# Kernel tuning notes

Measured on AMD Instinct MI355X. Metric: run time of the kernel, lower is better.

The kernel has to match this reference:

```python
import jax, jax.numpy as jnp
import numpy as np

N = 20000      # num nodes
E = 320000     # num edges (avg degree 16)
R = 8          # num relations
D = 256        # input_dim / hidden dim
L = 6          # num_layers
EE = 32        # edge_embed_dim
B = 64         # batch size
K = 32         # num_negative + 1


def _layer_norm(x, g, b, eps=1e-5):
    mu = jnp.mean(x, axis=-1, keepdims=True)
    var = jnp.var(x, axis=-1, keepdims=True)
    return (x - mu) * jax.lax.rsqrt(var + eps) * g + b


def setup_inputs() -> dict:
    key = jax.random.key(0)
    ks = jax.random.split(key, 10)
    edge_index = jax.random.randint(ks[0], (2, E), 0, N)
    edge_type = jax.random.randint(ks[1], (E,), 0, R)
    edge_embed = jax.random.normal(ks[2], (E, EE), dtype=jnp.float32)
    src = jax.random.randint(ks[3], (B, K), 0, N)
    tgt = jax.random.randint(ks[4], (B, K), 0, N)
    rel = jax.random.randint(ks[5], (B, K), 0, R)
    batch = jnp.stack([src, tgt, rel], axis=-1)  # [B, K, 3]
    s = 1.0 / np.sqrt(D)
    W = jax.random.normal(ks[6], (L, R, D, D), dtype=jnp.float32) * s      # per-relation weights
    Wself = jax.random.normal(ks[7], (L, D, D), dtype=jnp.float32) * s     # self-loop weights
    We = jax.random.normal(ks[8], (L, EE, D), dtype=jnp.float32) * (1.0 / np.sqrt(EE))  # edge-embed proj (stage add)
    gamma = jnp.ones((L, D), dtype=jnp.float32)
    beta = jnp.zeros((L, D), dtype=jnp.float32)
    rel_emb = jax.random.normal(ks[9], (R, D), dtype=jnp.float32) * s      # DistMult relation embedding
    return dict(edge_index=edge_index, edge_type=edge_type, edge_embed=edge_embed,
                batch=batch, W=W, Wself=Wself, We=We, gamma=gamma, beta=beta,
                rel_emb=rel_emb)


def reference(edge_index, edge_type, edge_embed, batch, W, Wself, We, gamma, beta, rel_emb):
    src, dst = edge_index[0], edge_index[1]
    # mean aggregation denominator: in-degree per node (over all relations)
    deg = jnp.clip(jax.ops.segment_sum(jnp.ones((E,), jnp.float32), dst, num_segments=N), 1.0)
    # segment id combining relation and destination node -> aggregate-then-transform trick
    seg = edge_type * N + dst
    x = jnp.ones((N, D), dtype=jnp.float32)
    for l in range(L):
        # stage 'add': message = x[src] + proj(edge_embed)
        msg = x[src] + edge_embed @ We[l]                                  # [E, D]
        agg = jax.ops.segment_sum(msg, seg, num_segments=R * N).reshape(R, N, D)
        h = jnp.einsum('rnd,rdf->nf', agg, W[l]) / deg[:, None] + x @ Wself[l]
        h = jax.nn.relu(_layer_norm(h, gamma[l], beta[l]))
        x = h + x  # short_cut residual
    # DistMult scoring: gather source/target/relation embeddings, mul, sum
    s_emb = x[batch[..., 0]]          # [B, K, D]
    t_emb = x[batch[..., 1]]          # [B, K, D]
    r_emb = rel_emb[batch[..., 2]]    # [B, K, D]
    return jnp.sum(s_emb * r_emb * t_emb, axis=-1)  # [B, K]
```

## Files before the change

### kernel.cpp

```cpp
#include <hip/hip_runtime.h>
#include <hip/hip_bf16.h>

#define NN 20000
#define NP 20032
#define NE 320000
#define RR 8
#define DD 256
#define LL 6
#define EED 32
#define BB 64
#define KK 32
#define MM (NN * RR)
#define NSB 79
#define NB2 626
#define HSTR 260
#define ES_CAP 1280

typedef __bf16 bf8 __attribute__((ext_vector_type(8)));
typedef float f4 __attribute__((ext_vector_type(4)));

__device__ inline float lo2f(unsigned v) { return __uint_as_float(v << 16); }
__device__ inline float hi2f(unsigned v) { return __uint_as_float(v & 0xffff0000u); }
__device__ inline unsigned short f2bf(float f) {
    unsigned u = __float_as_uint(f);
    return (unsigned short)((u + 0x7fff + ((u >> 16) & 1)) >> 16);
}
__device__ inline unsigned pack2(float lo, float hi) {
    return (unsigned)f2bf(lo) | ((unsigned)f2bf(hi) << 16);
}


__global__ __launch_bounds__(256) void hist_kernel(const int* __restrict__ dstv,
                                                   const int* __restrict__ typev,
                                                   int* __restrict__ hist) {
    int e = blockIdx.x * 256 + threadIdx.x;
    if (e < NE) atomicAdd(&hist[dstv[e] * 8 + typev[e]], 1);
}

__global__ __launch_bounds__(256) void scan1_kernel(const int* __restrict__ hist,
                                                    int* __restrict__ excl,
                                                    int* __restrict__ bsums) {
    __shared__ int tmp[256];
    int tid = threadIdx.x;
    int base = blockIdx.x * 2048 + tid * 8;
    int v[8]; int s = 0;
#pragma unroll
    for (int i = 0; i < 8; ++i) {
        v[i] = (base + i < MM) ? hist[base + i] : 0;
        s += v[i];
    }
    tmp[tid] = s;
    __syncthreads();
    for (int off = 1; off < 256; off <<= 1) {
        int t = (tid >= off) ? tmp[tid - off] : 0;
        __syncthreads();
        tmp[tid] += t;
        __syncthreads();
    }
    int run = tmp[tid] - s;
#pragma unroll
    for (int i = 0; i < 8; ++i) {
        if (base + i < MM) excl[base + i] = run;
        run += v[i];
    }
    if (tid == 255) bsums[blockIdx.x] = tmp[255];
}

__global__ __launch_bounds__(128) void scan2_kernel(int* __restrict__ bsums) {
    __shared__ int tmp[128];
    int tid = threadIdx.x;
    int orig = (tid < NSB) ? bsums[tid] : 0;
    tmp[tid] = orig;
    __syncthreads();
    for (int off = 1; off < 128; off <<= 1) {
        int t = (tid >= off) ? tmp[tid - off] : 0;
        __syncthreads();
        tmp[tid] += t;
        __syncthreads();
    }
    if (tid < NSB) bsums[tid] = tmp[tid] - orig;
}

__global__ __launch_bounds__(256) void add_off_kernel(const int* __restrict__ excl,
                                                      const int* __restrict__ bsums,
                                                      int* __restrict__ seg_start,
                                                      int* __restrict__ cursor) {
    int i = blockIdx.x * 256 + threadIdx.x;
    if (i < MM) {
        int v = excl[i] + bsums[i >> 11];
        seg_start[i] = v;
        cursor[i] = v;
    }
    if (i == 0) seg_start[MM] = NE;
}

__global__ __launch_bounds__(256) void sort_scatter_kernel(
    const int* __restrict__ srcv, const int* __restrict__ dstv,
    const int* __restrict__ typev, int* __restrict__ cursor,
    int* __restrict__ esrc, int* __restrict__ eid) {
    int e = blockIdx.x * 256 + threadIdx.x;
    if (e < NE) {
        int key = dstv[e] * 8 + typev[e];
        int pos = atomicAdd(&cursor[key], 1);
        esrc[pos] = srcv[e];
        eid[pos]  = e;
    }
}

__global__ __launch_bounds__(256) void invdeg_kernel(const int* __restrict__ seg_start,
                                                     float* __restrict__ invdeg) {
    int i = blockIdx.x * 256 + threadIdx.x;
    if (i < NN) {
        int d = seg_start[i * 8 + 8] - seg_start[i * 8];
        invdeg[i] = 1.0f / (float)max(d, 1);
    }
}


__global__ __launch_bounds__(256) void eagg_kernel(
    const int* __restrict__ seg_start, const int* __restrict__ eid,
    const float* __restrict__ ee, const float* __restrict__ invdeg,
    unsigned short* __restrict__ eaggbf) {
    int tid = threadIdx.x;
    int s = blockIdx.x * 8 + (tid >> 5);
    int j = tid & 31;
    int n = s >> 3, r = s & 7;
    int j0 = seg_start[s], j1 = seg_start[s + 1];
    float sum = 0.0f;
    for (int p = j0; p < j1; ++p)
        sum += ee[eid[p] * EED + j];
    eaggbf[(size_t)n * DD + r * EED + j] = f2bf(sum * invdeg[n]);
}

__global__ __launch_bounds__(256) void whe_kernel(const float* __restrict__ We,
                                                  const float* __restrict__ W,
                                                  float* __restrict__ Whe) {
    __shared__ float WeS[EED * 32];
    int b = blockIdx.x;
    int l = b >> 6;
    int r = (b >> 3) & 7;
    int dc = b & 7;
    int tid = threadIdx.x;
    {
        int j = tid >> 3, dl = (tid & 7) * 4;
        *(float4*)&WeS[j * 32 + dl] =
            *(const float4*)&We[(size_t)l * EED * DD + (size_t)j * DD + dc * 32 + dl];
    }
    __syncthreads();
    const float* Wr = W + ((size_t)l * 8 + r) * DD * DD + (size_t)dc * 32 * DD;
    float acc[EED];
#pragma unroll
    for (int j = 0; j < EED; ++j) acc[j] = 0.0f;
    for (int dl = 0; dl < 32; ++dl) {
        float w = Wr[(size_t)dl * DD + tid];
#pragma unroll
        for (int j = 0; j < EED; ++j) acc[j] += WeS[j * 32 + dl] * w;
    }
    float* outp = Whe + (size_t)l * DD * DD + r * EED * DD + tid;
#pragma unroll
    for (int j = 0; j < EED; ++j) unsafeAtomicAdd(&outp[j * DD], acc[j]);
}

__global__ __launch_bounds__(256) void bswz_kernel(const float* __restrict__ W,
                                                   const float* __restrict__ Wself,
                                                   const float* __restrict__ Whe,
                                                   unsigned short* __restrict__ Bsw) {
    int gid = blockIdx.x * 256 + threadIdx.x;
    int f = gid & 255;
    int t = gid >> 8;
    int quad = t & 3; t >>= 2;
    int kb = t & 7; t >>= 3;
    int p = t % 10, l = t / 10;
    const float* base = (p == 0) ? Wself + (size_t)l * DD * DD
                      : (p <= 8) ? W + ((size_t)l * 8 + (p - 1)) * DD * DD
                                 : Whe + (size_t)l * DD * DD;
    int k0 = kb * 32 + quad * 8;
    unsigned pk[4];
#pragma unroll
    for (int jj = 0; jj < 4; ++jj)
        pk[jj] = pack2(base[(size_t)(k0 + 2 * jj) * DD + f],
                       base[(size_t)(k0 + 2 * jj + 1) * DD + f]);
    uint4 v = make_uint4(pk[0], pk[1], pk[2], pk[3]);
    *(uint4*)&Bsw[(size_t)gid * 8] = v;
}

__global__ __launch_bounds__(256) void init_x_kernel(float* __restrict__ x,
                                                     unsigned short* __restrict__ xbf) {
    int i = blockIdx.x * 256 + threadIdx.x;
    ((float4*)x)[i] = make_float4(1.f, 1.f, 1.f, 1.f);
    ((uint2*)xbf)[i] = make_uint2(0x3f803f80u, 0x3f803f80u);
}

__global__ __launch_bounds__(512, 2) void fused_layer_kernel(
    const int* __restrict__ seg_start, const int* __restrict__ esrc,
    const unsigned short* __restrict__ xbf, const unsigned short* __restrict__ eaggbf,
    const unsigned short* __restrict__ Bswl, const float* __restrict__ xin,
    const float* __restrict__ gl, const float* __restrict__ bl,
    float* __restrict__ xout, unsigned short* __restrict__ xbfout) {
    __shared__ __align__(16) unsigned char smem[32768 + 1040 + ES_CAP * 4];
    float* Hs = (float*)smem;
    int* boundsS = (int*)(smem + 32768);
    int* esrcS   = (int*)(smem + 32768 + 1040);
    int tid = threadIdx.x;
    int wave = tid >> 6, lane = tid & 63;
    bool consumer = wave < 4;
    int cwave = wave & 3;
    int row0 = blockIdx.x * 32;
    int m = lane & 15, quad = lane >> 4;
    int colg = lane >> 1, half = lane & 1, cofs = lane * 4;
    f4 acc[2][4] = {};

    if (tid < 257) {
        int idx = row0 * 8 + tid;
        boundsS[tid] = (idx <= MM) ? seg_start[idx] : NE;
    }
    uint4 xs[2];
#pragma unroll
    for (int c = 0; c < 2; ++c) {
        int i = tid + c * 512;
        int row = i >> 5, sc = i & 31;
        xs[c] = *(const uint4*)&xbf[(size_t)(row0 + row) * DD + sc * 8];
    }
    __syncthreads();
    int blk0 = boundsS[0];
    int blkE = boundsS[256] - blk0;
    for (int j = tid; j < ES_CAP; j += 512)
        esrcS[j] = (j < blkE) ? esrc[blk0 + j] : 0;
#pragma unroll
    for (int c = 0; c < 2; ++c) {
        int i = tid + c * 512;
        int row = i >> 5, sc = i & 31;
        *(uint4*)&smem[row * 512 + ((sc ^ row) * 16)] = xs[c];
    }
    bf8 breg[2][4];
    if (consumer) {
#pragma unroll
        for (int nt = 0; nt < 4; ++nt) {
            breg[0][nt] = *(const bf8*)&Bswl[((size_t)quad * 256 + cwave * 64 + nt * 16 + m) * 8];
            breg[1][nt] = *(const bf8*)&Bswl[((size_t)(4 + quad) * 256 + cwave * 64 + nt * 16 + m) * 8];
        }
    }
    __syncthreads();

    for (int p = 0; p < 10; ++p) {
        unsigned char* bufp = smem + (p & 1) * 16384;
        unsigned char* bufn = smem + ((p + 1) & 1) * 16384;
        if (consumer) {
#pragma unroll
            for (int kb = 0; kb < 8; ++kb) {
                bf8 afr[2];
#pragma unroll
                for (int mt = 0; mt < 2; ++mt) {
                    int rowl = mt * 16 + m;
                    afr[mt] = *(bf8*)&bufp[rowl * 512 + (((kb * 4 + quad) ^ rowl) * 16)];
                }
#pragma unroll
                for (int mt = 0; mt < 2; ++mt)
#pragma unroll
                    for (int nt = 0; nt < 4; ++nt)
                        acc[mt][nt] = __builtin_amdgcn_mfma_f32_16x16x32_bf16(
                            afr[mt], breg[kb & 1][nt], acc[mt][nt], 0, 0, 0);
                int gn = p * 8 + kb + 2;
                if (gn < 80) {
#pragma unroll
                    for (int nt = 0; nt < 4; ++nt)
                        breg[kb & 1][nt] = *(const bf8*)&Bswl[((size_t)gn * 4 + quad) * 2048
                                                              + ((size_t)(cwave * 64 + nt * 16 + m)) * 8];
                }
            }
        } else if (p < 8) {
#pragma unroll
            for (int grp = 0; grp < 2; ++grp) {
                int jj0[4], jj1[4], dg[4];
#pragma unroll
                for (int i = 0; i < 4; ++i) {
                    int nl = cwave * 8 + grp * 4 + i;
                    jj0[i] = boundsS[nl * 8 + p] - blk0;
                    jj1[i] = boundsS[nl * 8 + p + 1] - blk0;
                    dg[i]  = boundsS[nl * 8 + 8] - boundsS[nl * 8];
                }
                int srcq[4][4];
#pragma unroll
                for (int i = 0; i < 4; ++i)
#pragma unroll
                    for (int q = 0; q < 4; ++q) {
                        int jc = jj0[i] + q;
                        jc = (jc < ES_CAP) ? jc : (ES_CAP - 1);
                        srcq[i][q] = esrcS[jc];
                    }
                uint2 gv[4][4];
#pragma unroll
                for (int i = 0; i < 4; ++i)
#pragma unroll
                    for (int q = 0; q < 4; ++q)
                        gv[i][q] = *(const uint2*)&xbf[(size_t)srcq[i][q] * DD + cofs];
#pragma unroll
                for (int i = 0; i < 4; ++i) {
                    int nl = cwave * 8 + grp * 4 + i;
                    int j0 = jj0[i], j1 = jj1[i];
                    float a0 = 0.f, a1 = 0.f, a2 = 0.f, a3 = 0.f;
#pragma unroll
                    for (int q = 0; q < 4; ++q) {
                        unsigned vx = (j0 + q < j1) ? gv[i][q].x : 0u;
                        unsigned vy = (j0 + q < j1) ? gv[i][q].y : 0u;
                        a0 += lo2f(vx); a1 += hi2f(vx);
                        a2 += lo2f(vy); a3 += hi2f(vy);
                    }
                    for (int j = j0 + 4; j < j1; ++j) {
                        int src = (j < ES_CAP) ? esrcS[j] : esrc[blk0 + j];
                        uint2 v = *(const uint2*)&xbf[(size_t)src * DD + cofs];
                        a0 += lo2f(v.x); a1 += hi2f(v.x);
                        a2 += lo2f(v.y); a3 += hi2f(v.y);
                    }
                    float idg = 1.0f / (float)max(dg[i], 1);
                    uint2 o = make_uint2(pack2(a0 * idg, a1 * idg), pack2(a2 * idg, a3 * idg));
                    *(uint2*)&bufn[nl * 512 + ((colg ^ nl) * 16) + half * 8] = o;
                }
            }
        } else if (p == 8) {
#pragma unroll
            for (int it = 0; it < 4; ++it) {
                int row = cwave * 8 + it * 2 + (lane >> 5);
                int sc = lane & 31;
                uint4 v = *(const uint4*)&eaggbf[(size_t)(row0 + row) * DD + sc * 8];
                *(uint4*)&bufn[row * 512 + ((sc ^ row) * 16)] = v;
            }
        }
        __syncthreads();
    }

    float4 xvr[4];
#pragma unroll
    for (int rr = 0; rr < 4; ++rr) {
        int row = wave * 4 + rr;
        xvr[rr] = *(const float4*)&xin[(size_t)(row0 + row) * DD + lane * 4];
    }
    float4 g  = *(const float4*)&gl[lane * 4];
    float4 bb = *(const float4*)&bl[lane * 4];
    if (consumer) {
#pragma unroll
        for (int mt = 0; mt < 2; ++mt)
#pragma unroll
            for (int nt = 0; nt < 4; ++nt)
#pragma unroll
                for (int rg = 0; rg < 4; ++rg)
                    Hs[(mt * 16 + quad * 4 + rg) * HSTR + cwave * 64 + nt * 16 + m] = acc[mt][nt][rg];
    }
    __syncthreads();
#pragma unroll
    for (int rr = 0; rr < 4; ++rr) {
        int row = wave * 4 + rr;
        float4 v = *(float4*)&Hs[row * HSTR + lane * 4];
        float s = v.x + v.y + v.z + v.w;
        float q = v.x * v.x + v.y * v.y + v.z * v.z + v.w * v.w;
#pragma unroll
        for (int off = 32; off; off >>= 1) {
            s += __shfl_xor(s, off);
            q += __shfl_xor(q, off);
        }
        float mu  = s * (1.0f / DD);
        float var = q * (1.0f / DD) - mu * mu;
        float rs  = rsqrtf(var + 1e-5f);
        size_t xi = (size_t)(row0 + row) * DD + lane * 4;
        float4 xv = xvr[rr];
        float4 o;
        o.x = fmaxf((v.x - mu) * rs * g.x + bb.x, 0.0f) + xv.x;
        o.y = fmaxf((v.y - mu) * rs * g.y + bb.y, 0.0f) + xv.y;
        o.z = fmaxf((v.z - mu) * rs * g.z + bb.z, 0.0f) + xv.z;
        o.w = fmaxf((v.w - mu) * rs * g.w + bb.w, 0.0f) + xv.w;
        *(float4*)&xout[xi] = o;
        *(uint2*)&xbfout[xi] = make_uint2(pack2(o.x, o.y), pack2(o.z, o.w));
    }
}

__global__ __launch_bounds__(256) void score_kernel(
    const int* __restrict__ batch, const float* __restrict__ x,
    const float* __restrict__ rel_emb, float* __restrict__ out) {
    int tid = threadIdx.x;
    int wave = tid >> 6, lane = tid & 63;
    int idx = blockIdx.x * 4 + wave;
    int s = batch[idx * 3 + 0], t = batch[idx * 3 + 1], r = batch[idx * 3 + 2];
    float4 sv = *(const float4*)&x[(size_t)s * DD + lane * 4];
    float4 tv = *(const float4*)&x[(size_t)t * DD + lane * 4];
    float4 rv = *(const float4*)&rel_emb[(size_t)r * DD + lane * 4];
    float sum = sv.x * rv.x * tv.x + sv.y * rv.y * tv.y +
                sv.z * rv.z * tv.z + sv.w * rv.w * tv.w;
#pragma unroll
    for (int off = 32; off; off >>= 1) sum += __shfl_xor(sum, off);
    if (lane == 0) out[idx] = sum;
}

extern "C" void kernel_launch(void* const* d_in, const int* in_sizes, int n_in,
                              void* d_out, int out_size, void* d_ws, size_t ws_size,
                              hipStream_t stream) {
    const int*   edge_index = (const int*)d_in[0];
    const int*   srcv   = edge_index;
    const int*   dstv   = edge_index + NE;
    const int*   typev  = (const int*)d_in[1];
    const float* ee     = (const float*)d_in[2];
    const int*   batch  = (const int*)d_in[3];
    const float* W      = (const float*)d_in[4];
    const float* Wself  = (const float*)d_in[5];
    const float* We     = (const float*)d_in[6];
    const float* gamma  = (const float*)d_in[7];
    const float* beta   = (const float*)d_in[8];
    const float* rel_emb= (const float*)d_in[9];
    float* out = (float*)d_out;

    float* xA     = (float*)d_ws;
    float* xB     = xA + (size_t)NP * DD;
    float* Whe    = xB + (size_t)NP * DD;
    float* invdeg = Whe + (size_t)LL * DD * DD;
    unsigned short* xbfA   = (unsigned short*)(invdeg + NN);
    unsigned short* xbfB   = xbfA + (size_t)NP * DD;
    unsigned short* eaggbf = xbfB + (size_t)NP * DD;
    unsigned short* Bsw    = eaggbf + (size_t)NP * DD;
    int* hist      = (int*)(Bsw + (size_t)LL * 2560 * DD);
    int* excl      = hist + MM;
    int* seg_start = excl + MM;
    int* cursor    = seg_start + MM + 1;
    int* bsums     = cursor + MM;
    int* esrc      = bsums + 256;
    int* eid       = esrc + NE;

    hipMemsetAsync(hist, 0, MM * sizeof(int), stream);
    hist_kernel<<<(NE + 255) / 256, 256, 0, stream>>>(dstv, typev, hist);
    scan1_kernel<<<NSB, 256, 0, stream>>>(hist, excl, bsums);
    scan2_kernel<<<1, 128, 0, stream>>>(bsums);
    add_off_kernel<<<(MM + 255) / 256, 256, 0, stream>>>(excl, bsums, seg_start, cursor);
    invdeg_kernel<<<(NN + 255) / 256, 256, 0, stream>>>(seg_start, invdeg);
    sort_scatter_kernel<<<(NE + 255) / 256, 256, 0, stream>>>(srcv, dstv, typev, cursor, esrc, eid);

    eagg_kernel<<<MM / 8, 256, 0, stream>>>(seg_start, eid, ee, invdeg, eaggbf);
    hipMemsetAsync(Whe, 0, (size_t)LL * DD * DD * sizeof(float), stream);
    whe_kernel<<<LL * 64, 256, 0, stream>>>(We, W, Whe);
    bswz_kernel<<<LL * 10 * 8 * 4, 256, 0, stream>>>(W, Wself, Whe, Bsw);
    init_x_kernel<<<(NP * DD / 4) / 256, 256, 0, stream>>>(xA, xbfA);

    float* xin = xA;  float* xout = xB;
    unsigned short* xbin = xbfA;  unsigned short* xbout = xbfB;
    for (int l = 0; l < LL; ++l) {
        fused_layer_kernel<<<NB2, 512, 0, stream>>>(seg_start, esrc, xbin, eaggbf,
            Bsw + (size_t)l * 2560 * DD, xin,
            gamma + (size_t)l * DD, beta + (size_t)l * DD, xout, xbout);
        float* t = xin; xin = xout; xout = t;
        unsigned short* tb = xbin; xbin = xbout; xbout = tb;
    }
    score_kernel<<<(BB * KK) / 4, 256, 0, stream>>>(batch, xin, rel_emb, out);
}
```

Measured before the change: 894.2 us.

## Software-pipeline neighbor gathers across relation phases and preload edge aggregate

Producer waves now prefetch the next relation's first four neighbor rows into registers while reducing the current relation, instead of issuing and waiting on each group's gathers inside its phase. The edge-embedding aggregate is loaded into a third shared buffer before the main loop, and per-node inverse degrees are precomputed. The loop is fully unrolled and __syncthreads is replaced by a raw barrier that waits only on LDS counters. Launch bounds now ask for 4 blocks per CU, which with 48KB+ of shared memory and a large register footprint (gv[8][4]) may cause spills or be unachievable.

```diff
diff --git a/kernel.cpp b/kernel.cpp
--- a/kernel.cpp
+++ b/kernel.cpp
@@ -191,16 +191,16 @@
     ((uint2*)xbf)[i] = make_uint2(0x3f803f80u, 0x3f803f80u);
 }
 
-__global__ __launch_bounds__(512, 2) void fused_layer_kernel(
+__global__ __launch_bounds__(512, 4) void fused_layer_kernel(
     const int* __restrict__ seg_start, const int* __restrict__ esrc,
     const unsigned short* __restrict__ xbf, const unsigned short* __restrict__ eaggbf,
     const unsigned short* __restrict__ Bswl, const float* __restrict__ xin,
     const float* __restrict__ gl, const float* __restrict__ bl,
     float* __restrict__ xout, unsigned short* __restrict__ xbfout) {
-    __shared__ __align__(16) unsigned char smem[32768 + 1040 + ES_CAP * 4];
+    __shared__ __align__(16) unsigned char smem[49152 + 1040 + ES_CAP * 4];
     float* Hs = (float*)smem;
-    int* boundsS = (int*)(smem + 32768);
-    int* esrcS   = (int*)(smem + 32768 + 1040);
+    int* boundsS = (int*)(smem + 49152);
+    int* esrcS   = (int*)(smem + 49152 + 1040);
     int tid = threadIdx.x;
     int wave = tid >> 6, lane = tid & 63;
     bool consumer = wave < 4;
@@ -221,6 +221,15 @@
         int row = i >> 5, sc = i & 31;
         xs[c] = *(const uint4*)&xbf[(size_t)(row0 + row) * DD + sc * 8];
     }
+    uint4 ev[4];
+    if (!consumer) {
+#pragma unroll
+        for (int it = 0; it < 4; ++it) {
+            int row = cwave * 8 + it * 2 + (lane >> 5);
+            int sc = lane & 31;
+            ev[it] = *(const uint4*)&eaggbf[(size_t)(row0 + row) * DD + sc * 8];
+        }
+    }
     __syncthreads();
     int blk0 = boundsS[0];
     int blkE = boundsS[256] - blk0;
@@ -232,6 +241,23 @@
         int row = i >> 5, sc = i & 31;
         *(uint4*)&smem[row * 512 + ((sc ^ row) * 16)] = xs[c];
     }
+    int jroll[8];
+    float idgr[8];
+    if (!consumer) {
+#pragma unroll
+        for (int it = 0; it < 4; ++it) {
+            int row = cwave * 8 + it * 2 + (lane >> 5);
+            int sc = lane & 31;
+            *(uint4*)&smem[32768 + row * 512 + ((sc ^ row) * 16)] = ev[it];
+        }
+#pragma unroll
+        for (int i8 = 0; i8 < 8; ++i8) {
+            int nl = cwave * 8 + i8;
+            jroll[i8] = boundsS[nl * 8] - blk0;
+            int dg = boundsS[nl * 8 + 8] - boundsS[nl * 8];
+            idgr[i8] = 1.0f / (float)max(dg, 1);
+        }
+    }
     bf8 breg[2][4];
     if (consumer) {
 #pragma unroll
@@ -242,10 +268,23 @@
     }
     __syncthreads();
 
+    uint2 gv[8][4];
+    if (!consumer) {
+#pragma unroll
+        for (int i8 = 0; i8 < 8; ++i8) {
+#pragma unroll
+            for (int s = 0; s < 4; ++s) {
+                int jc = jroll[i8] + s;
+                jc = (jc < ES_CAP) ? jc : (ES_CAP - 1);
+                gv[i8][s] = *(const uint2*)&xbf[(size_t)esrcS[jc] * DD + cofs];
+            }
+        }
+    }
+
+#pragma unroll
     for (int p = 0; p < 10; ++p) {
-        unsigned char* bufp = smem + (p & 1) * 16384;
-        unsigned char* bufn = smem + ((p + 1) & 1) * 16384;
         if (consumer) {
+            unsigned char* bufp = smem + ((p == 9) ? 2 : (p & 1)) * 16384;
 #pragma unroll
             for (int kb = 0; kb < 8; ++kb) {
                 bf8 afr[2];
@@ -269,64 +308,44 @@
                 }
             }
         } else if (p < 8) {
-#pragma unroll
-            for (int grp = 0; grp < 2; ++grp) {
-                int jj0[4], jj1[4], dg[4];
-#pragma unroll
-                for (int i = 0; i < 4; ++i) {
-                    int nl = cwave * 8 + grp * 4 + i;
-                    jj0[i] = boundsS[nl * 8 + p] - blk0;
-                    jj1[i] = boundsS[nl * 8 + p + 1] - blk0;
-                    dg[i]  = boundsS[nl * 8 + 8] - boundsS[nl * 8];
+            int q = p + 1;
+            unsigned char* bufn = smem + ((q & 1) * 16384);
+#pragma unroll
+            for (int i8 = 0; i8 < 8; ++i8) {
+                int nl = cwave * 8 + i8;
+                int j0 = jroll[i8];
+                int j1 = boundsS[nl * 8 + q] - blk0;
+                float a0 = 0.f, a1 = 0.f, a2 = 0.f, a3 = 0.f;
+#pragma unroll
+                for (int s = 0; s < 4; ++s) {
+                    unsigned vx = (j0 + s < j1) ? gv[i8][s].x : 0u;
+                    unsigned vy = (j0 + s < j1) ? gv[i8][s].y : 0u;
+                    a0 += lo2f(vx); a1 += hi2f(vx);
+                    a2 += lo2f(vy); a3 += hi2f(vy);
                 }
-                int srcq[4][4];
-#pragma unroll
-                for (int i = 0; i < 4; ++i)
-#pragma unroll
-                    for (int q = 0; q < 4; ++q) {
-                        int jc = jj0[i] + q;
+                if (q < 8) {
+#pragma unroll
+                    for (int s = 0; s < 4; ++s) {
+                        int jc = j1 + s;
                         jc = (jc < ES_CAP) ? jc : (ES_CAP - 1);
-                        srcq[i][q] = esrcS[jc];
+                        gv[i8][s] = *(const uint2*)&xbf[(size_t)esrcS[jc] * DD + cofs];
                     }
-                uint2 gv[4][4];
-#pragma unroll
-                for (int i = 0; i < 4; ++i)
-#pragma unroll
-                    for (int q = 0; q < 4; ++q)
-                        gv[i][q] = *(const uint2*)&xbf[(size_t)srcq[i][q] * DD + cofs];
-#pragma unroll
-                for (int i = 0; i < 4; ++i) {
-                    int nl = cwave * 8 + grp * 4 + i;
-                    int j0 = jj0[i], j1 = jj1[i];
-                    float a0 = 0.f, a1 = 0.f, a2 = 0.f, a3 = 0.f;
-#pragma unroll
-                    for (int q = 0; q < 4; ++q) {
-                        unsigned vx = (j0 + q < j1) ? gv[i][q].x : 0u;
-                        unsigned vy = (j0 + q < j1) ? gv[i][q].y : 0u;
-                        a0 += lo2f(vx); a1 += hi2f(vx);
-                        a2 += lo2f(vy); a3 += hi2f(vy);
-                    }
-                    for (int j = j0 + 4; j < j1; ++j) {
-                        int src = (j < ES_CAP) ? esrcS[j] : esrc[blk0 + j];
-                        uint2 v = *(const uint2*)&xbf[(size_t)src * DD + cofs];
-                        a0 += lo2f(v.x); a1 += hi2f(v.x);
-                        a2 += lo2f(v.y); a3 += hi2f(v.y);
-                    }
-                    float idg = 1.0f / (float)max(dg[i], 1);
-                    uint2 o = make_uint2(pack2(a0 * idg, a1 * idg), pack2(a2 * idg, a3 * idg));
-                    *(uint2*)&bufn[nl * 512 + ((colg ^ nl) * 16) + half * 8] = o;
                 }
+                for (int j = j0 + 4; j < j1; ++j) {
+                    int src = (j < ES_CAP) ? esrcS[j] : esrc[blk0 + j];
+                    uint2 v = *(const uint2*)&xbf[(size_t)src * DD + cofs];
+                    a0 += lo2f(v.x); a1 += hi2f(v.x);
+                    a2 += lo2f(v.y); a3 += hi2f(v.y);
+                }
+                float idg = idgr[i8];
+                *(uint2*)&bufn[nl * 512 + ((colg ^ nl) * 16) + half * 8] =
+                    make_uint2(pack2(a0 * idg, a1 * idg), pack2(a2 * idg, a3 * idg));
+                jroll[i8] = j1;
             }
-        } else if (p == 8) {
-#pragma unroll
-            for (int it = 0; it < 4; ++it) {
-                int row = cwave * 8 + it * 2 + (lane >> 5);
-                int sc = lane & 31;
-                uint4 v = *(const uint4*)&eaggbf[(size_t)(row0 + row) * DD + sc * 8];
-                *(uint4*)&bufn[row * 512 + ((sc ^ row) * 16)] = v;
-            }
-        }
-        __syncthreads();
+        }
+        asm volatile("s_waitcnt lgkmcnt(0)" ::: "memory");
+        __builtin_amdgcn_s_barrier();
+        __builtin_amdgcn_sched_barrier(0);
     }
 
     float4 xvr[4];
```

Measured after the change: 2.421 ms. 2.71x slower.

## Merge producer and consumer waves so every wave gathers and runs MFMA

Applied to the files above, without the earlier changes.

Drops the warp specialization in which four waves gathered neighbour rows while four ran MFMAs. Now all eight waves do both: each wave gathers four nodes with software-prefetched gather loads carried across phases, then computes a 32-column slice of the output. A raw s_barrier with an explicit lgkmcnt wait replaces __syncthreads. The aim is to double MFMA and gather parallelism per block and hide gather latency by issuing the next phase's loads early, at the cost of more live registers and lost overlap between specialized roles.

```diff
diff --git a/kernel.cpp b/kernel.cpp
--- a/kernel.cpp
+++ b/kernel.cpp
@@ -202,13 +202,11 @@
     int* boundsS = (int*)(smem + 32768);
     int* esrcS   = (int*)(smem + 32768 + 1040);
     int tid = threadIdx.x;
-    int wave = tid >> 6, lane = tid & 63;
-    bool consumer = wave < 4;
-    int cwave = wave & 3;
+    int wv = tid >> 6, lane = tid & 63;
     int row0 = blockIdx.x * 32;
     int m = lane & 15, quad = lane >> 4;
     int colg = lane >> 1, half = lane & 1, cofs = lane * 4;
-    f4 acc[2][4] = {};
+    f4 acc[2][2] = {};
 
     if (tid < 257) {
         int idx = row0 * 8 + tid;
@@ -232,124 +230,126 @@
         int row = i >> 5, sc = i & 31;
         *(uint4*)&smem[row * 512 + ((sc ^ row) * 16)] = xs[c];
     }
-    bf8 breg[2][4];
-    if (consumer) {
-#pragma unroll
-        for (int nt = 0; nt < 4; ++nt) {
-            breg[0][nt] = *(const bf8*)&Bswl[((size_t)quad * 256 + cwave * 64 + nt * 16 + m) * 8];
-            breg[1][nt] = *(const bf8*)&Bswl[((size_t)(4 + quad) * 256 + cwave * 64 + nt * 16 + m) * 8];
+    int jroll[4];
+    float idgr[4];
+#pragma unroll
+    for (int i4 = 0; i4 < 4; ++i4) {
+        int nl = wv * 4 + i4;
+        jroll[i4] = boundsS[nl * 8] - blk0;
+        int dg = boundsS[nl * 8 + 8] - boundsS[nl * 8];
+        idgr[i4] = 1.0f / (float)max(dg, 1);
+    }
+    bf8 breg[2][2];
+#pragma unroll
+    for (int nt = 0; nt < 2; ++nt) {
+        breg[0][nt] = *(const bf8*)&Bswl[((size_t)quad * 256 + wv * 32 + nt * 16 + m) * 8];
+        breg[1][nt] = *(const bf8*)&Bswl[((size_t)(4 + quad) * 256 + wv * 32 + nt * 16 + m) * 8];
+    }
+    __syncthreads();
+
+    uint2 gv[4][4];
+#pragma unroll
+    for (int i4 = 0; i4 < 4; ++i4)
+#pragma unroll
+        for (int s = 0; s < 4; ++s) {
+            int jc = jroll[i4] + s;
+            jc = (jc < ES_CAP) ? jc : (ES_CAP - 1);
+            gv[i4][s] = *(const uint2*)&xbf[(size_t)esrcS[jc] * DD + cofs];
         }
-    }
-    __syncthreads();
-
+
+#pragma unroll 1
     for (int p = 0; p < 10; ++p) {
         unsigned char* bufp = smem + (p & 1) * 16384;
         unsigned char* bufn = smem + ((p + 1) & 1) * 16384;
-        if (consumer) {
-#pragma unroll
-            for (int kb = 0; kb < 8; ++kb) {
-                bf8 afr[2];
-#pragma unroll
-                for (int mt = 0; mt < 2; ++mt) {
-                    int rowl = mt * 16 + m;
-                    afr[mt] = *(bf8*)&bufp[rowl * 512 + (((kb * 4 + quad) ^ rowl) * 16)];
+        if (p < 8) {
+#pragma unroll
+            for (int i4 = 0; i4 < 4; ++i4) {
+                int nl = wv * 4 + i4;
+                int j0 = jroll[i4];
+                int j1 = boundsS[nl * 8 + p + 1] - blk0;
+                float a0 = 0.f, a1 = 0.f, a2 = 0.f, a3 = 0.f;
+#pragma unroll
+                for (int s = 0; s < 4; ++s) {
+                    unsigned vx = (j0 + s < j1) ? gv[i4][s].x : 0u;
+                    unsigned vy = (j0 + s < j1) ? gv[i4][s].y : 0u;
+                    a0 += lo2f(vx); a1 += hi2f(vx);
+                    a2 += lo2f(vy); a3 += hi2f(vy);
                 }
-#pragma unroll
-                for (int mt = 0; mt < 2; ++mt)
-#pragma unroll
-                    for (int nt = 0; nt < 4; ++nt)
-                        acc[mt][nt] = __builtin_amdgcn_mfma_f32_16x16x32_bf16(
-                            afr[mt], breg[kb & 1][nt], acc[mt][nt], 0, 0, 0);
-                int gn = p * 8 + kb + 2;
-                if (gn < 80) {
-#pragma unroll
-                    for (int nt = 0; nt < 4; ++nt)
-                        breg[kb & 1][nt] = *(const bf8*)&Bswl[((size_t)gn * 4 + quad) * 2048
-                                                              + ((size_t)(cwave * 64 + nt * 16 + m)) * 8];
+                if (p < 7) {
+#pragma unroll
+                    for (int s = 0; s < 4; ++s) {
+                        int jc = j1 + s;
+                        jc = (jc < ES_CAP) ? jc : (ES_CAP - 1);
+                        gv[i4][s] = *(const uint2*)&xbf[(size_t)esrcS[jc] * DD + cofs];
+                    }
+                } else {
+                    gv[i4][0] = *(const uint2*)&eaggbf[(size_t)(row0 + nl) * DD + cofs];
                 }
-            }
-        } else if (p < 8) {
-#pragma unroll
-            for (int grp = 0; grp < 2; ++grp) {
-                int jj0[4], jj1[4], dg[4];
-#pragma unroll
-                for (int i = 0; i < 4; ++i) {
-                    int nl = cwave * 8 + grp * 4 + i;
-                    jj0[i] = boundsS[nl * 8 + p] - blk0;
-                    jj1[i] = boundsS[nl * 8 + p + 1] - blk0;
-                    dg[i]  = boundsS[nl * 8 + 8] - boundsS[nl * 8];
+                for (int j = j0 + 4; j < j1; ++j) {
+                    int src = (j < ES_CAP) ? esrcS[j] : esrc[blk0 + j];
+                    uint2 v = *(const uint2*)&xbf[(size_t)src * DD + cofs];
+                    a0 += lo2f(v.x); a1 += hi2f(v.x);
+                    a2 += lo2f(v.y); a3 += hi2f(v.y);
                 }
-                int srcq[4][4];
-#pragma unroll
-                for (int i = 0; i < 4; ++i)
-#pragma unroll
-                    for (int q = 0; q < 4; ++q) {
-                        int jc = jj0[i] + q;
-                        jc = (jc < ES_CAP) ? jc : (ES_CAP - 1);
-                        srcq[i][q] = esrcS[jc];
-                    }
-                uint2 gv[4][4];
-#pragma unroll
-                for (int i = 0; i < 4; ++i)
-#pragma unroll
-                    for (int q = 0; q < 4; ++q)
-                        gv[i][q] = *(const uint2*)&xbf[(size_t)srcq[i][q] * DD + cofs];
-#pragma unroll
-                for (int i = 0; i < 4; ++i) {
-                    int nl = cwave * 8 + grp * 4 + i;
-                    int j0 = jj0[i], j1 = jj1[i];
-                    float a0 = 0.f, a1 = 0.f, a2 = 0.f, a3 = 0.f;
-#pragma unroll
-                    for (int q = 0; q < 4; ++q) {
-                        unsigned vx = (j0 + q < j1) ? gv[i][q].x : 0u;
-                        unsigned vy = (j0 + q < j1) ? gv[i][q].y : 0u;
-                        a0 += lo2f(vx); a1 += hi2f(vx);
-                        a2 += lo2f(vy); a3 += hi2f(vy);
-                    }
-                    for (int j = j0 + 4; j < j1; ++j) {
-                        int src = (j < ES_CAP) ? esrcS[j] : esrc[blk0 + j];
-                        uint2 v = *(const uint2*)&xbf[(size_t)src * DD + cofs];
-                        a0 += lo2f(v.x); a1 += hi2f(v.x);
-                        a2 += lo2f(v.y); a3 += hi2f(v.y);
-                    }
-                    float idg = 1.0f / (float)max(dg[i], 1);
-                    uint2 o = make_uint2(pack2(a0 * idg, a1 * idg), pack2(a2 * idg, a3 * idg));
-                    *(uint2*)&bufn[nl * 512 + ((colg ^ nl) * 16) + half * 8] = o;
-                }
+                float idg = idgr[i4];
+                *(uint2*)&bufn[nl * 512 + ((colg ^ nl) * 16) + half * 8] =
+                    make_uint2(pack2(a0 * idg, a1 * idg), pack2(a2 * idg, a3 * idg));
+                jroll[i4] = j1;
             }
         } else if (p == 8) {
 #pragma unroll
-            for (int it = 0; it < 4; ++it) {
-                int row = cwave * 8 + it * 2 + (lane >> 5);
-                int sc = lane & 31;
-                uint4 v = *(const uint4*)&eaggbf[(size_t)(row0 + row) * DD + sc * 8];
-                *(uint4*)&bufn[row * 512 + ((sc ^ row) * 16)] = v;
+            for (int i4 = 0; i4 < 4; ++i4) {
+                int nl = wv * 4 + i4;
+                *(uint2*)&bufn[nl * 512 + ((colg ^ nl) * 16) + half * 8] = gv[i4][0];
             }
         }
-        __syncthreads();
+#pragma unroll
+        for (int kb = 0; kb < 8; ++kb) {
+            bf8 afr[2];
+#pragma unroll
+            for (int mt = 0; mt < 2; ++mt) {
+                int rowl = mt * 16 + m;
+                afr[mt] = *(bf8*)&bufp[rowl * 512 + (((kb * 4 + quad) ^ rowl) * 16)];
+            }
+#pragma unroll
+            for (int mt = 0; mt < 2; ++mt)
+#pragma unroll
+                for (int nt = 0; nt < 2; ++nt)
+                    acc[mt][nt] = __builtin_amdgcn_mfma_f32_16x16x32_bf16(
+                        afr[mt], breg[kb & 1][nt], acc[mt][nt], 0, 0, 0);
+            int gn = p * 8 + kb + 2;
+            if (gn < 80) {
+#pragma unroll
+                for (int nt = 0; nt < 2; ++nt)
+                    breg[kb & 1][nt] = *(const bf8*)&Bswl[((size_t)gn * 4 + quad) * 2048
+                                                          + ((size_t)(wv * 32 + nt * 16 + m)) * 8];
+            }
+        }
+        __builtin_amdgcn_sched_barrier(0);
+        asm volatile("s_waitcnt lgkmcnt(0)");
+        __builtin_amdgcn_s_barrier();
+        __builtin_amdgcn_sched_barrier(0);
     }
 
     float4 xvr[4];
 #pragma unroll
     for (int rr = 0; rr < 4; ++rr) {
-        int row = wave * 4 + rr;
+        int row = wv * 4 + rr;
         xvr[rr] = *(const float4*)&xin[(size_t)(row0 + row) * DD + lane * 4];
     }
     float4 g  = *(const float4*)&gl[lane * 4];
     float4 bb = *(const float4*)&bl[lane * 4];
-    if (consumer) {
-#pragma unroll
-        for (int mt = 0; mt < 2; ++mt)
-#pragma unroll
-            for (int nt = 0; nt < 4; ++nt)
-#pragma unroll
-                for (int rg = 0; rg < 4; ++rg)
-                    Hs[(mt * 16 + quad * 4 + rg) * HSTR + cwave * 64 + nt * 16 + m] = acc[mt][nt][rg];
-    }
+#pragma unroll
+    for (int mt = 0; mt < 2; ++mt)
+#pragma unroll
+        for (int nt = 0; nt < 2; ++nt)
+#pragma unroll
+            for (int rg = 0; rg < 4; ++rg)
+                Hs[(mt * 16 + quad * 4 + rg) * HSTR + wv * 32 + nt * 16 + m] = acc[mt][nt][rg];
     __syncthreads();
 #pragma unroll
     for (int rr = 0; rr < 4; ++rr) {
-        int row = wave * 4 + rr;
+        int row = wv * 4 + rr;
         float4 v = *(float4*)&Hs[row * HSTR + lane * 4];
         float s = v.x + v.y + v.z + v.w;
         float q = v.x * v.x + v.y * v.y + v.z * v.z + v.w * v.w;
```

After: 1.008 ms. 12.8% more time.
